# Optimization experiments

Measured on AMD Instinct MI355X. Metric: run time of the kernel, lower is better.

## Reference

```python
import jax, jax.numpy as jnp
import numpy as np

B, N, DIM, H = 2, 4096, 1024, 16
LAT = 1024
CTX = N - LAT            # 3072 context tokens
SEG = 12                 # num_segments
CHUNK = CTX // SEG       # 256 tokens per segment
D = DIM // H             # 64 head dim
SCALE = D ** -0.5
LN_EPS = 1e-5
NEG = float(-np.finfo(np.float32).max)


def _split_heads(t):  # [B, N, DIM] -> [(B*H), N, D]
    return t.reshape(B, N, H, D).transpose(0, 2, 1, 3).reshape(B * H, N, D)


def _merge_heads(t):  # [(B*H), n, D] -> [B, n, DIM]
    n = t.shape[1]
    return t.reshape(B, H, n, D).transpose(0, 2, 1, 3).reshape(B, n, DIM)


def _layernorm(t, g, b):  # LN over last dim (head dim)
    mu = t.mean(-1, keepdims=True)
    var = ((t - mu) ** 2).mean(-1, keepdims=True)
    return (t - mu) * jax.lax.rsqrt(var + LN_EPS) * g + b


def _rope(t):  # rotary embedding over full head dim, half-split rotate
    pos = jnp.arange(N, dtype=jnp.float32)
    inv = 1.0 / (10000.0 ** (jnp.arange(0, D, 2, dtype=jnp.float32) / D))
    freqs = pos[:, None] * inv[None, :]          # [N, D/2]
    emb = jnp.concatenate([freqs, freqs], -1)    # [N, D]
    cos, sin = jnp.cos(emb), jnp.sin(emb)
    rot = jnp.concatenate([-t[..., D // 2:], t[..., : D // 2]], -1)
    return t * cos + rot * sin


def setup_inputs() -> dict:
    key = jax.random.key(0)
    ks = jax.random.split(key, 4)
    s = 0.02
    return {
        "x": jax.random.normal(ks[0], (B, N, DIM), jnp.float32),
        "Wq": jax.random.normal(ks[1], (DIM, DIM), jnp.float32) * s,
        "Wkv": jax.random.normal(ks[2], (DIM, DIM), jnp.float32) * s,
        "Wo": jax.random.normal(ks[3], (DIM, DIM), jnp.float32) * s,
        "bo": jnp.zeros((DIM,), jnp.float32),
        "ln_g": jnp.ones((D,), jnp.float32),
        "ln_b": jnp.zeros((D,), jnp.float32),
    }


def reference(x, Wq, Wkv, Wo, bo, ln_g, ln_b):
    q = _split_heads(x @ Wq)    # [(BH), N, D]
    kv = _split_heads(x @ Wkv)  # [(BH), N, D]
    q, kv = _rope(q), _rope(kv)

    lkv = _layernorm(kv, ln_g, ln_b)  # normalized keys/values, full seq

    q_lat = q[:, CTX:] * SCALE                                   # [(BH), LAT, D]
    q_ctx = (q[:, :CTX] * SCALE).reshape(B * H, SEG, CHUNK, D)   # segmented ctx queries
    lkv_ctx = lkv[:, :CTX].reshape(B * H, SEG, CHUNK, D)         # segmented norm'd kv

    # latent queries: full attention over all N positions, causal among latents
    lsim = jnp.einsum('bid,bjd->bij', q_lat, lkv)                # [(BH), LAT, N]
    tri = jnp.triu(jnp.ones((LAT, LAT), bool), 1)
    lat_block = jnp.where(tri, NEG, lsim[:, :, CTX:])
    lsim = jnp.concatenate([lsim[:, :, :CTX], lat_block], axis=-1)
    attn = jax.nn.softmax(lsim, axis=-1)
    out_lat = jnp.einsum('bij,bjd->bid', attn, lkv)              # [(BH), LAT, D]

    # context queries: block-diagonal segmented local attention (non-causal)
    sim_ctx = jnp.einsum('bsid,bsjd->bsij', q_ctx, lkv_ctx)      # [(BH), SEG, CHUNK, CHUNK]
    attn_ctx = jax.nn.softmax(sim_ctx, axis=-1)
    out_ctx = jnp.einsum('bsij,bsjd->bsid', attn_ctx, lkv_ctx).reshape(B * H, CTX, D)

    out = jnp.concatenate([_merge_heads(out_ctx), _merge_heads(out_lat)], axis=1)
    return out @ Wo + bo
```

## Files before the change

kernel.cpp:

```cpp
#include <hip/hip_runtime.h>
#include <math.h>

#define NB_B 2
#define NB_N 4096
#define NB_DIM 1024
#define NB_H 16
#define NB_D 64
#define NB_CTX 3072
#define NSPLIT 4
#define QSCALE 0.18033688011112042f
#define NEGF -3.0e38f

typedef __attribute__((ext_vector_type(8))) short short8;
typedef __attribute__((ext_vector_type(4))) short s4v;
typedef __attribute__((ext_vector_type(4))) float f32x4;

#if __has_builtin(__builtin_amdgcn_mfma_f32_16x16x16bf16_1k)
__device__ __forceinline__ f32x4 mfma16(s4v a, s4v b, f32x4 c) {
  return __builtin_amdgcn_mfma_f32_16x16x16bf16_1k(a, b, c, 0, 0, 0);
}
#else
__device__ __forceinline__ f32x4 mfma16(s4v a, s4v b, f32x4 c) {
  f32x4 d;
  asm volatile("v_mfma_f32_16x16x16_bf16 %0, %1, %2, %3"
               : "=v"(d) : "v"(a), "v"(b), "v"(c));
  return d;
}
#endif

__device__ __forceinline__ unsigned short f2bf(float f) {
  union { float f; unsigned u; } v; v.f = f;
  unsigned r = v.u + 0x7fffu + ((v.u >> 16) & 1u);
  return (unsigned short)(r >> 16);
}

__device__ __forceinline__ void async16(const void* g, void* l) {
  typedef const unsigned int __attribute__((address_space(1)))* gas_t;
  typedef unsigned int __attribute__((address_space(3)))* las_t;
  __builtin_amdgcn_global_load_lds((gas_t)(unsigned long long)g,
                                   (las_t)(unsigned)(unsigned long long)l,
                                   16, 0, 0);
}

__global__ __launch_bounds__(256) void k_prep(
    const float* __restrict__ x,
    const float* __restrict__ Wq, const float* __restrict__ Wkv, const float* __restrict__ Wo,
    unsigned short* __restrict__ xb, unsigned short* __restrict__ WqkvT,
    unsigned short* __restrict__ WoT, float2* __restrict__ tab)
{
  __shared__ float tile[64][65];
  const int bx = blockIdx.x, tid = threadIdx.x;
  if (bx < 2048) {
    const float4* x4 = (const float4*)x;
    ushort4* xb4 = (ushort4*)xb;
    const int n4 = (NB_B * NB_N * NB_DIM) / 4;
    for (int i = bx * 256 + tid; i < n4; i += 2048 * 256) {
      float4 v = x4[i];
      ushort4 o;
      o.x = f2bf(v.x); o.y = f2bf(v.y); o.z = f2bf(v.z); o.w = f2bf(v.w);
      xb4[i] = o;
    }
  } else if (bx < 2816) {
    int idx = bx - 2048;
    int z = idx >> 8, rem = idx & 255;
    const float* W; unsigned short* out;
    if (z == 0)      { W = Wq;  out = WqkvT; }
    else if (z == 1) { W = Wkv; out = WqkvT + 1024 * 1024; }
    else             { W = Wo;  out = WoT; }
    int c0 = (rem & 15) * 64, k0 = (rem >> 4) * 64;
    int tx = tid & 63, ty = tid >> 6;
    #pragma unroll
    for (int i = 0; i < 16; ++i) {
      int k = ty + i * 4;
      tile[k][tx] = W[(long)(k0 + k) * 1024 + c0 + tx];
    }
    __syncthreads();
    #pragma unroll
    for (int i = 0; i < 16; ++i) {
      int c = ty + i * 4;
      out[(long)(c0 + c) * 1024 + k0 + tx] = f2bf(tile[tx][c]);
    }
  } else {
    int idx = (bx - 2816) * 256 + tid;
    int n = idx >> 5, fi = idx & 31;
    float inv = exp2f(-(float)fi * (13.287712379549449f / 32.0f));
    float ang = (float)n * inv;
    float s, c;
    sincosf(ang, &s, &c);
    tab[idx] = make_float2(c, s);
  }
}

__global__ __launch_bounds__(256) void k_gemm_qkv(
    const unsigned short* __restrict__ A,
    const unsigned short* __restrict__ Bt,
    unsigned short* __restrict__ qf,
    unsigned short* __restrict__ lkvp,
    const float2* __restrict__ tab,
    const float* __restrict__ ln_g,
    const float* __restrict__ ln_b)
{
  __shared__ unsigned short As[128 * 32];
  __shared__ unsigned short Bs[128 * 32];
  const int tid = threadIdx.x;
  const int w = tid >> 6, lane = tid & 63;
  const int wr = w >> 1, wc = w & 1;
  const int quad = lane >> 4, l15 = lane & 15;
  const long tm = (long)blockIdx.y * 128, tn = (long)blockIdx.x * 128;
  const int K = 1024;

  f32x4 acc[4][4];
  #pragma unroll
  for (int i = 0; i < 4; ++i)
    #pragma unroll
    for (int j = 0; j < 4; ++j)
      acc[i][j] = (f32x4){0.f, 0.f, 0.f, 0.f};

  const unsigned short* Ag0 = A + (tm + w * 16 + (lane >> 2)) * K + (lane & 3) * 8;
  const unsigned short* Bg0 = Bt + (tn + w * 16 + (lane >> 2)) * K + (lane & 3) * 8;
  const unsigned short* Ag1 = Ag0 + (long)64 * K;
  const unsigned short* Bg1 = Bg0 + (long)64 * K;
  unsigned short* Al0 = &As[(w * 16) * 32];
  unsigned short* Al1 = &As[(64 + w * 16) * 32];
  unsigned short* Bl0 = &Bs[(w * 16) * 32];
  unsigned short* Bl1 = &Bs[(64 + w * 16) * 32];

  for (int k0 = 0; k0 < K; k0 += 32) {
    __syncthreads();
    async16(Ag0 + k0, Al0);
    async16(Ag1 + k0, Al1);
    async16(Bg0 + k0, Bl0);
    async16(Bg1 + k0, Bl1);
    __syncthreads();
    short8 af[4], bfr[4];
    #pragma unroll
    for (int i = 0; i < 4; ++i)
      af[i] = *(const short8*)&As[(wr * 64 + i * 16 + l15) * 32 + quad * 8];
    #pragma unroll
    for (int j = 0; j < 4; ++j)
      bfr[j] = *(const short8*)&Bs[(wc * 64 + j * 16 + l15) * 32 + quad * 8];
    #pragma unroll
    for (int i = 0; i < 4; ++i)
      #pragma unroll
      for (int j = 0; j < 4; ++j)
        acc[i][j] = __builtin_amdgcn_mfma_f32_16x16x32_bf16(af[i], bfr[j], acc[i][j], 0, 0, 0);
  }

  const int col_base = (int)tn + wc * 64;
  const bool is_q = col_base < 1024;
  const int hh = (col_base & 1023) >> 6;
  unsigned short* dst = is_q ? qf : lkvp;
  float g_ln[4], b_ln[4];
  #pragma unroll
  for (int j = 0; j < 4; ++j) { g_ln[j] = ln_g[j * 16 + l15]; b_ln[j] = ln_b[j * 16 + l15]; }

  const int row_base = (int)tm + wr * 64;
  #pragma unroll
  for (int i = 0; i < 4; ++i) {
    #pragma unroll
    for (int r = 0; r < 4; ++r) {
      const int row = row_base + i * 16 + quad * 4 + r;
      const int n = row & 4095, b = row >> 12;
      const float2 cs0 = tab[n * 32 + l15];
      const float2 cs1 = tab[n * 32 + 16 + l15];
      float val[4];
      #pragma unroll
      for (int j = 0; j < 4; ++j) {
        float t = acc[i][j][r], pt = acc[i][j ^ 2][r];
        float2 cs = (j & 1) ? cs1 : cs0;
        float rot = (j < 2) ? -pt : pt;
        val[j] = t * cs.x + rot * cs.y;
      }
      unsigned short* orow = dst + ((long)(b * 16 + hh) * NB_N + n) * 64;
      if (is_q) {
        #pragma unroll
        for (int j = 0; j < 4; ++j)
          orow[j * 16 + l15] = f2bf(val[j] * QSCALE);
      } else {
        float s = val[0] + val[1] + val[2] + val[3];
        #pragma unroll
        for (int o = 1; o < 16; o <<= 1) s += __shfl_xor(s, o);
        const float mu = s * 0.015625f;
        float dv[4], vs = 0.f;
        #pragma unroll
        for (int j = 0; j < 4; ++j) { dv[j] = val[j] - mu; vs += dv[j] * dv[j]; }
        #pragma unroll
        for (int o = 1; o < 16; o <<= 1) vs += __shfl_xor(vs, o);
        const float rr = rsqrtf(vs * 0.015625f + 1e-5f);
        #pragma unroll
        for (int j = 0; j < 4; ++j)
          orow[j * 16 + l15] = f2bf(dv[j] * rr * g_ln[j] + b_ln[j]);
      }
    }
  }
}

__global__ __launch_bounds__(256) void k_gemm_bt(
    const unsigned short* __restrict__ A,
    const unsigned short* __restrict__ Bt,
    float* __restrict__ C,
    const float* __restrict__ bias,
    int K, int ldc)
{
  __shared__ unsigned short As[128 * 32];
  __shared__ unsigned short Bs[128 * 32];
  const int tid = threadIdx.x;
  const int w = tid >> 6, lane = tid & 63;
  const int wr = w >> 1, wc = w & 1;
  const int quad = lane >> 4, l15 = lane & 15;
  const long tm = (long)blockIdx.y * 128, tn = (long)blockIdx.x * 128;

  f32x4 acc[4][4];
  #pragma unroll
  for (int i = 0; i < 4; ++i)
    #pragma unroll
    for (int j = 0; j < 4; ++j)
      acc[i][j] = (f32x4){0.f, 0.f, 0.f, 0.f};

  const unsigned short* Ag0 = A + (tm + w * 16 + (lane >> 2)) * K + (lane & 3) * 8;
  const unsigned short* Bg0 = Bt + (tn + w * 16 + (lane >> 2)) * K + (lane & 3) * 8;
  const unsigned short* Ag1 = Ag0 + (long)64 * K;
  const unsigned short* Bg1 = Bg0 + (long)64 * K;
  unsigned short* Al0 = &As[(w * 16) * 32];
  unsigned short* Al1 = &As[(64 + w * 16) * 32];
  unsigned short* Bl0 = &Bs[(w * 16) * 32];
  unsigned short* Bl1 = &Bs[(64 + w * 16) * 32];

  for (int k0 = 0; k0 < K; k0 += 32) {
    __syncthreads();
    async16(Ag0 + k0, Al0);
    async16(Ag1 + k0, Al1);
    async16(Bg0 + k0, Bl0);
    async16(Bg1 + k0, Bl1);
    __syncthreads();
    short8 af[4], bfr[4];
    #pragma unroll
    for (int i = 0; i < 4; ++i)
      af[i] = *(const short8*)&As[(wr * 64 + i * 16 + l15) * 32 + quad * 8];
    #pragma unroll
    for (int j = 0; j < 4; ++j)
      bfr[j] = *(const short8*)&Bs[(wc * 64 + j * 16 + l15) * 32 + quad * 8];
    #pragma unroll
    for (int i = 0; i < 4; ++i)
      #pragma unroll
      for (int j = 0; j < 4; ++j)
        acc[i][j] = __builtin_amdgcn_mfma_f32_16x16x32_bf16(af[i], bfr[j], acc[i][j], 0, 0, 0);
  }

  #pragma unroll
  for (int j = 0; j < 4; ++j) {
    const long col = tn + wc * 64 + j * 16 + l15;
    const float bv = bias ? bias[col] : 0.0f;
    #pragma unroll
    for (int i = 0; i < 4; ++i) {
      #pragma unroll
      for (int r = 0; r < 4; ++r) {
        const long row = tm + wr * 64 + i * 16 + quad * 4 + r;
        C[row * ldc + col] = acc[i][j][r] + bv;
      }
    }
  }
}

__global__ __launch_bounds__(256) void k_attn(
    const unsigned short* __restrict__ qf,
    const unsigned short* __restrict__ lkv,
    unsigned short* __restrict__ attn_out,
    float* __restrict__ Opart,
    float* __restrict__ mpart,
    float* __restrict__ lpart)
{
  __shared__ unsigned short smem[18432];
  unsigned short* QPs = smem + 9216;
  float* smf = (float*)smem;

  const int tid = threadIdx.x;
  const int w = tid >> 6, lane = tid & 63;
  const int quad = lane >> 4, l15 = lane & 15;

  const int bx = blockIdx.x;
  int bh, q0tok, kstart, kt0, kt1, q0lat, s6 = 0, qb = 0;
  bool latent;
  if (bx < 256 * NSPLIT) {
    latent = true;
    qb = bx / NSPLIT;
    s6 = bx % NSPLIT;
    bh = qb >> 3;
    q0lat = (qb & 7) * 128;
    q0tok = NB_CTX + q0lat;
    kstart = 0;
    int nkt = (NB_CTX + q0lat + 128) >> 6;
    kt0 = (s6 * nkt) / NSPLIT;
    kt1 = ((s6 + 1) * nkt) / NSPLIT;
  } else {
    latent = false;
    int idx = bx - 256 * NSPLIT;
    bh = idx / 24;
    int r2 = idx % 24;
    int seg = r2 >> 1;
    q0lat = 0;
    q0tok = seg * 256 + (r2 & 1) * 128;
    kstart = seg * 256;
    kt0 = 0; kt1 = 4;
  }

  const unsigned short* qbase = qf + ((long)bh * NB_N + q0tok) * 64;
  const unsigned short* kbase = lkv + (long)bh * NB_N * 64;

  const int skey = tid >> 3, sdc = tid & 7;

  uint4 gA, gB;
  {
    const int key0 = kstart + kt0 * 64;
    gA = *(const uint4*)(kbase + (long)(key0 + skey) * 64 + sdc * 8);
    gB = *(const uint4*)(kbase + (long)(key0 + skey + 32) * 64 + sdc * 8);
  }

  #pragma unroll
  for (int p = 0; p < 4; ++p) {
    int ci = p * 256 + tid;
    int row = ci >> 3, dc = ci & 7;
    *(uint4*)&QPs[row * 72 + dc * 8] = *(const uint4*)(qbase + row * 64 + dc * 8);
  }

  {
    unsigned short* Ks = smem;
    unsigned short* Vt = smem + 4608;
    *(uint4*)&Ks[skey * 72 + sdc * 8] = gA;
    *(uint4*)&Ks[(skey + 32) * 72 + sdc * 8] = gB;
    const unsigned short* eA = (const unsigned short*)&gA;
    const unsigned short* eB = (const unsigned short*)&gB;
    const int swA = skey ^ (sdc * 8);
    const int swB = (skey + 32) ^ (sdc * 8);
    #pragma unroll
    for (int j = 0; j < 8; ++j) {
      Vt[(sdc * 8 + j) * 72 + swA] = eA[j];
      Vt[(sdc * 8 + j) * 72 + swB] = eB[j];
    }
  }
  __syncthreads();

  short8 qfr[2][2];
  #pragma unroll
  for (int qg = 0; qg < 2; ++qg)
    #pragma unroll
    for (int kc = 0; kc < 2; ++kc)
      qfr[qg][kc] = *(const short8*)&QPs[(w * 32 + qg * 16 + l15) * 72 + kc * 32 + quad * 8];
  __syncthreads();

  f32x4 ot[2][4];
  float mi[2], li[2];
  #pragma unroll
  for (int qg = 0; qg < 2; ++qg) {
    #pragma unroll
    for (int dt = 0; dt < 4; ++dt) ot[qg][dt] = (f32x4){0.f, 0.f, 0.f, 0.f};
    mi[qg] = NEGF; li[qg] = 0.f;
  }

  for (int kt = kt0; kt < kt1; ++kt) {
    const int cur = (kt - kt0) & 1;
    unsigned short* Ks = smem + cur * 9216;
    unsigned short* Vt = Ks + 4608;
    const int key0 = kstart + kt * 64;
    const bool more = (kt + 1 < kt1);

    if (more) {
      const int key0n = key0 + 64;
      gA = *(const uint4*)(kbase + (long)(key0n + skey) * 64 + sdc * 8);
      gB = *(const uint4*)(kbase + (long)(key0n + skey + 32) * 64 + sdc * 8);
    }

    f32x4 st[2][4];
    #pragma unroll
    for (int qg = 0; qg < 2; ++qg)
      #pragma unroll
      for (int k4 = 0; k4 < 4; ++k4)
        st[qg][k4] = (f32x4){0.f, 0.f, 0.f, 0.f};
    #pragma unroll
    for (int kc = 0; kc < 2; ++kc) {
      short8 kf[4];
      #pragma unroll
      for (int k4 = 0; k4 < 4; ++k4)
        kf[k4] = *(const short8*)&Ks[(k4 * 16 + l15) * 72 + kc * 32 + quad * 8];
      #pragma unroll
      for (int qg = 0; qg < 2; ++qg)
        #pragma unroll
        for (int k4 = 0; k4 < 4; ++k4)
          st[qg][k4] = __builtin_amdgcn_mfma_f32_16x16x32_bf16(kf[k4], qfr[qg][kc], st[qg][k4], 0, 0, 0);
    }

    if (latent && key0 + 63 >= NB_CTX) {
      #pragma unroll
      for (int qg = 0; qg < 2; ++qg) {
        const int qrow = q0lat + w * 32 + qg * 16 + l15;
        #pragma unroll
        for (int k4 = 0; k4 < 4; ++k4)
          #pragma unroll
          for (int r = 0; r < 4; ++r) {
            const int kl = key0 + k4 * 16 + quad * 4 + r - NB_CTX;
            if (kl > qrow) st[qg][k4][r] = NEGF;
          }
      }
    }

    unsigned int pk[2][4][2];
    #pragma unroll
    for (int qg = 0; qg < 2; ++qg) {
      float mx = st[qg][0][0];
      #pragma unroll
      for (int k4 = 0; k4 < 4; ++k4)
        #pragma unroll
        for (int r = 0; r < 4; ++r) mx = fmaxf(mx, st[qg][k4][r]);
      mx = fmaxf(mx, __shfl_xor(mx, 16));
      mx = fmaxf(mx, __shfl_xor(mx, 32));
      const float mnew = fmaxf(mi[qg], mx);
      const float alpha = __builtin_amdgcn_exp2f(mi[qg] - mnew);
      mi[qg] = mnew;
      float rs = 0.f;
      #pragma unroll
      for (int k4 = 0; k4 < 4; ++k4) {
        unsigned int b[4];
        #pragma unroll
        for (int r = 0; r < 4; ++r) {
          float p = __builtin_amdgcn_exp2f(st[qg][k4][r] - mnew);
          unsigned int pb = __float_as_uint(p) & 0xffff0000u;
          rs += __uint_as_float(pb);
          b[r] = pb;
        }
        pk[qg][k4][0] = __builtin_amdgcn_perm(b[1], b[0], 0x07060302);
        pk[qg][k4][1] = __builtin_amdgcn_perm(b[3], b[2], 0x07060302);
      }
      rs += __shfl_xor(rs, 16);
      rs += __shfl_xor(rs, 32);
      li[qg] = li[qg] * alpha + rs;
      #pragma unroll
      for (int dt = 0; dt < 4; ++dt) {
        ot[qg][dt][0] *= alpha; ot[qg][dt][1] *= alpha;
        ot[qg][dt][2] *= alpha; ot[qg][dt][3] *= alpha;
      }
    }

    #pragma unroll
    for (int k4 = 0; k4 < 4; ++k4) {
      s4v vf[4];
      const int kb = k4 * 16 + quad * 4;
      #pragma unroll
      for (int dt = 0; dt < 4; ++dt) {
        const int row = dt * 16 + l15;
        vf[dt] = *(const s4v*)&Vt[row * 72 + (kb ^ (row & 56))];
      }
      #pragma unroll
      for (int qg = 0; qg < 2; ++qg) {
        s4v pf;
        ((unsigned int*)&pf)[0] = pk[qg][k4][0];
        ((unsigned int*)&pf)[1] = pk[qg][k4][1];
        #pragma unroll
        for (int dt = 0; dt < 4; ++dt)
          ot[qg][dt] = mfma16(vf[dt], pf, ot[qg][dt]);
      }
    }

    if (more) {
      unsigned short* Kn = smem + (cur ^ 1) * 9216;
      unsigned short* Vn = Kn + 4608;
      *(uint4*)&Kn[skey * 72 + sdc * 8] = gA;
      *(uint4*)&Kn[(skey + 32) * 72 + sdc * 8] = gB;
      const unsigned short* eA = (const unsigned short*)&gA;
      const unsigned short* eB = (const unsigned short*)&gB;
      const int swA = skey ^ (sdc * 8);
      const int swB = (skey + 32) ^ (sdc * 8);
      #pragma unroll
      for (int j = 0; j < 8; ++j) {
        Vn[(sdc * 8 + j) * 72 + swA] = eA[j];
        Vn[(sdc * 8 + j) * 72 + swB] = eB[j];
      }
    }
    __syncthreads();
  }

  if (latent && quad == 0) {
    const long pb = (long)(s6 * 256 + qb) * 128;
    #pragma unroll
    for (int qg = 0; qg < 2; ++qg) {
      mpart[pb + w * 32 + qg * 16 + l15] = mi[qg];
      lpart[pb + w * 32 + qg * 16 + l15] = li[qg];
    }
  }
  #pragma unroll
  for (int qg = 0; qg < 2; ++qg) {
    const int q = w * 32 + qg * 16 + l15;
    #pragma unroll
    for (int dt = 0; dt < 4; ++dt)
      #pragma unroll
      for (int r = 0; r < 4; ++r)
        smf[q * 68 + dt * 16 + quad * 4 + r] = ot[qg][dt][r];
    if (!latent && quad == 0) smf[q * 68 + 64] = li[qg];
  }
  __syncthreads();
  const int row = tid >> 1, half = tid & 1;
  if (latent) {
    const long pb = (long)(s6 * 256 + qb) * 128;
    float4* dst = (float4*)(Opart + (pb + row) * 64 + half * 32);
    #pragma unroll
    for (int v = 0; v < 8; ++v)
      dst[v] = *(const float4*)&smf[row * 68 + half * 32 + v * 4];
  } else {
    const int b_ = bh >> 4, h_ = bh & 15;
    const float inv = 1.0f / smf[row * 68 + 64];
    const long tok = q0tok + row;
    unsigned short* orow = attn_out + ((long)b_ * NB_N + tok) * NB_DIM + h_ * 64 + half * 32;
    #pragma unroll
    for (int v = 0; v < 8; ++v) {
      float4 t = *(const float4*)&smf[row * 68 + half * 32 + v * 4];
      ushort4 u;
      u.x = f2bf(t.x * inv); u.y = f2bf(t.y * inv);
      u.z = f2bf(t.z * inv); u.w = f2bf(t.w * inv);
      *(ushort4*)(orow + v * 4) = u;
    }
  }
}

__global__ __launch_bounds__(256) void k_combine(
    const float* __restrict__ Opart, const float* __restrict__ mpart,
    const float* __restrict__ lpart, unsigned short* __restrict__ attn_out)
{
  const int qb = blockIdx.x;
  const int bh = qb >> 3, qt = qb & 7;
  const int b = bh >> 4, h = bh & 15;
  const int row = threadIdx.x >> 1;
  const int dh = (threadIdx.x & 1) * 32;
  float m[NSPLIT], l[NSPLIT];
  float mstar = NEGF;
  #pragma unroll
  for (int s = 0; s < NSPLIT; ++s) {
    m[s] = mpart[(s * 256 + qb) * 128 + row];
    l[s] = lpart[(s * 256 + qb) * 128 + row];
    mstar = fmaxf(mstar, m[s]);
  }
  float wgt[NSPLIT]; float lsum = 0.f;
  #pragma unroll
  for (int s = 0; s < NSPLIT; ++s) {
    wgt[s] = __builtin_amdgcn_exp2f(m[s] - mstar);
    lsum += wgt[s] * l[s];
  }
  const float inv = 1.0f / lsum;
  float o[32];
  #pragma unroll
  for (int e = 0; e < 32; ++e) o[e] = 0.f;
  #pragma unroll
  for (int s = 0; s < NSPLIT; ++s) {
    const float4* Op = (const float4*)(Opart + (((long)(s * 256 + qb) * 128 + row) * 64 + dh));
    #pragma unroll
    for (int v = 0; v < 8; ++v) {
      float4 t = Op[v];
      o[v * 4 + 0] += wgt[s] * t.x; o[v * 4 + 1] += wgt[s] * t.y;
      o[v * 4 + 2] += wgt[s] * t.z; o[v * 4 + 3] += wgt[s] * t.w;
    }
  }
  const long tok = NB_CTX + qt * 128 + row;
  unsigned short* orow = attn_out + ((long)b * NB_N + tok) * NB_DIM + h * 64 + dh;
  #pragma unroll
  for (int e = 0; e < 32; e += 4) {
    ushort4 u;
    u.x = f2bf(o[e] * inv);     u.y = f2bf(o[e + 1] * inv);
    u.z = f2bf(o[e + 2] * inv); u.w = f2bf(o[e + 3] * inv);
    *(ushort4*)(orow + e) = u;
  }
}

extern "C" void kernel_launch(void* const* d_in, const int* in_sizes, int n_in,
                              void* d_out, int out_size, void* d_ws, size_t ws_size,
                              hipStream_t stream)
{
  const float* x    = (const float*)d_in[0];
  const float* Wq   = (const float*)d_in[1];
  const float* Wkv  = (const float*)d_in[2];
  const float* Wo   = (const float*)d_in[3];
  const float* bo   = (const float*)d_in[4];
  const float* ln_g = (const float*)d_in[5];
  const float* ln_b = (const float*)d_in[6];
  float* out = (float*)d_out;

  char* ws = (char*)d_ws;
  unsigned short* xb    = (unsigned short*)(ws);
  unsigned short* WqkvT = (unsigned short*)(ws + (size_t)(16 << 20));
  unsigned short* WoT   = (unsigned short*)(ws + (size_t)(20 << 20));
  float2*         tab   = (float2*)        (ws + (size_t)(22 << 20));
  unsigned short* qfb   = (unsigned short*)(ws + (size_t)(24 << 20));
  unsigned short* lkv   = (unsigned short*)(ws + (size_t)(40 << 20));
  unsigned short* aout  = (unsigned short*)(ws + (size_t)(56 << 20));
  float*          Opart = (float*)         (ws + (size_t)(72 << 20));
  float*          mpart = (float*)         (ws + (size_t)(112 << 20));
  float*          lpart = (float*)         (ws + (size_t)(113 << 20));

  hipLaunchKernelGGL(k_prep, dim3(3328), dim3(256), 0, stream,
                     x, Wq, Wkv, Wo, xb, WqkvT, WoT, tab);
  hipLaunchKernelGGL(k_gemm_qkv, dim3(16, 64), dim3(256), 0, stream,
                     xb, WqkvT, qfb, lkv, tab, ln_g, ln_b);
  hipLaunchKernelGGL(k_attn, dim3(256 * NSPLIT + 768), dim3(256), 0, stream,
                     qfb, lkv, aout, Opart, mpart, lpart);
  hipLaunchKernelGGL(k_combine, dim3(256), dim3(256), 0, stream,
                     Opart, mpart, lpart, aout);
  hipLaunchKernelGGL(k_gemm_bt, dim3(8, 64), dim3(256), 0, stream,
                     aout, WoT, out, bo, 1024, 1024);
}
```

Baseline: 298.9 us.

## Restructure attention kernel: single-buffered LDS, lazy softmax rescale, d-major partials

```diff
diff --git a/kernel.cpp b/kernel.cpp
--- a/kernel.cpp
+++ b/kernel.cpp
@@ -270,9 +270,9 @@
     float* __restrict__ mpart,
     float* __restrict__ lpart)
 {
-  __shared__ unsigned short smem[18432];
-  unsigned short* QPs = smem + 9216;
-  float* smf = (float*)smem;
+  __shared__ unsigned short smem[9216];
+  unsigned short* Ks = smem;
+  unsigned short* Vt = smem + 4608;
 
   const int tid = threadIdx.x;
   const int w = tid >> 6, lane = tid & 63;
@@ -307,46 +307,21 @@
   const unsigned short* qbase = qf + ((long)bh * NB_N + q0tok) * 64;
   const unsigned short* kbase = lkv + (long)bh * NB_N * 64;
 
-  const int skey = tid >> 3, sdc = tid & 7;
+  short8 qfr[2][2];
+  #pragma unroll
+  for (int qg = 0; qg < 2; ++qg)
+    #pragma unroll
+    for (int kc = 0; kc < 2; ++kc)
+      qfr[qg][kc] = *(const short8*)(qbase + (w * 32 + qg * 16 + l15) * 64 + kc * 32 + quad * 8);
+
+  const int kp = tid >> 3, sdc = tid & 7;
 
   uint4 gA, gB;
   {
     const int key0 = kstart + kt0 * 64;
-    gA = *(const uint4*)(kbase + (long)(key0 + skey) * 64 + sdc * 8);
-    gB = *(const uint4*)(kbase + (long)(key0 + skey + 32) * 64 + sdc * 8);
-  }
-
-  #pragma unroll
-  for (int p = 0; p < 4; ++p) {
-    int ci = p * 256 + tid;
-    int row = ci >> 3, dc = ci & 7;
-    *(uint4*)&QPs[row * 72 + dc * 8] = *(const uint4*)(qbase + row * 64 + dc * 8);
-  }
-
-  {
-    unsigned short* Ks = smem;
-    unsigned short* Vt = smem + 4608;
-    *(uint4*)&Ks[skey * 72 + sdc * 8] = gA;
-    *(uint4*)&Ks[(skey + 32) * 72 + sdc * 8] = gB;
-    const unsigned short* eA = (const unsigned short*)&gA;
-    const unsigned short* eB = (const unsigned short*)&gB;
-    const int swA = skey ^ (sdc * 8);
-    const int swB = (skey + 32) ^ (sdc * 8);
-    #pragma unroll
-    for (int j = 0; j < 8; ++j) {
-      Vt[(sdc * 8 + j) * 72 + swA] = eA[j];
-      Vt[(sdc * 8 + j) * 72 + swB] = eB[j];
-    }
-  }
-  __syncthreads();
-
-  short8 qfr[2][2];
-  #pragma unroll
-  for (int qg = 0; qg < 2; ++qg)
-    #pragma unroll
-    for (int kc = 0; kc < 2; ++kc)
-      qfr[qg][kc] = *(const short8*)&QPs[(w * 32 + qg * 16 + l15) * 72 + kc * 32 + quad * 8];
-  __syncthreads();
+    gA = *(const uint4*)(kbase + (long)(key0 + 2 * kp) * 64 + sdc * 8);
+    gB = *(const uint4*)(kbase + (long)(key0 + 2 * kp + 1) * 64 + sdc * 8);
+  }
 
   f32x4 ot[2][4];
   float mi[2], li[2];
@@ -354,20 +329,29 @@
   for (int qg = 0; qg < 2; ++qg) {
     #pragma unroll
     for (int dt = 0; dt < 4; ++dt) ot[qg][dt] = (f32x4){0.f, 0.f, 0.f, 0.f};
-    mi[qg] = NEGF; li[qg] = 0.f;
+    mi[qg] = 0.f; li[qg] = 0.f;
   }
 
   for (int kt = kt0; kt < kt1; ++kt) {
-    const int cur = (kt - kt0) & 1;
-    unsigned short* Ks = smem + cur * 9216;
-    unsigned short* Vt = Ks + 4608;
     const int key0 = kstart + kt * 64;
-    const bool more = (kt + 1 < kt1);
-
-    if (more) {
+    __syncthreads();
+    *(uint4*)&Ks[(2 * kp) * 72 + sdc * 8] = gA;
+    *(uint4*)&Ks[(2 * kp + 1) * 72 + sdc * 8] = gB;
+    {
+      const unsigned short* eA = (const unsigned short*)&gA;
+      const unsigned short* eB = (const unsigned short*)&gB;
+      #pragma unroll
+      for (int j = 0; j < 8; ++j) {
+        const int d = sdc * 8 + j;
+        const unsigned int pair = (unsigned int)eA[j] | ((unsigned int)eB[j] << 16);
+        *(unsigned int*)&Vt[d * 72 + ((2 * kp) ^ (d & 56))] = pair;
+      }
+    }
+    __syncthreads();
+    if (kt + 1 < kt1) {
       const int key0n = key0 + 64;
-      gA = *(const uint4*)(kbase + (long)(key0n + skey) * 64 + sdc * 8);
-      gB = *(const uint4*)(kbase + (long)(key0n + skey + 32) * 64 + sdc * 8);
+      gA = *(const uint4*)(kbase + (long)(key0n + 2 * kp) * 64 + sdc * 8);
+      gB = *(const uint4*)(kbase + (long)(key0n + 2 * kp + 1) * 64 + sdc * 8);
     }
 
     f32x4 st[2][4];
@@ -404,25 +388,18 @@
     }
 
     unsigned int pk[2][4][2];
+    float tmx[2], trs[2];
     #pragma unroll
     for (int qg = 0; qg < 2; ++qg) {
+      float rs = 0.f;
       float mx = st[qg][0][0];
-      #pragma unroll
-      for (int k4 = 0; k4 < 4; ++k4)
-        #pragma unroll
-        for (int r = 0; r < 4; ++r) mx = fmaxf(mx, st[qg][k4][r]);
-      mx = fmaxf(mx, __shfl_xor(mx, 16));
-      mx = fmaxf(mx, __shfl_xor(mx, 32));
-      const float mnew = fmaxf(mi[qg], mx);
-      const float alpha = __builtin_amdgcn_exp2f(mi[qg] - mnew);
-      mi[qg] = mnew;
-      float rs = 0.f;
       #pragma unroll
       for (int k4 = 0; k4 < 4; ++k4) {
         unsigned int b[4];
         #pragma unroll
         for (int r = 0; r < 4; ++r) {
-          float p = __builtin_amdgcn_exp2f(st[qg][k4][r] - mnew);
+          mx = fmaxf(mx, st[qg][k4][r]);
+          float p = __builtin_amdgcn_exp2f(st[qg][k4][r] - mi[qg]);
           unsigned int pb = __float_as_uint(p) & 0xffff0000u;
           rs += __uint_as_float(pb);
           b[r] = pb;
@@ -430,14 +407,7 @@
         pk[qg][k4][0] = __builtin_amdgcn_perm(b[1], b[0], 0x07060302);
         pk[qg][k4][1] = __builtin_amdgcn_perm(b[3], b[2], 0x07060302);
       }
-      rs += __shfl_xor(rs, 16);
-      rs += __shfl_xor(rs, 32);
-      li[qg] = li[qg] * alpha + rs;
-      #pragma unroll
-      for (int dt = 0; dt < 4; ++dt) {
-        ot[qg][dt][0] *= alpha; ot[qg][dt][1] *= alpha;
-        ot[qg][dt][2] *= alpha; ot[qg][dt][3] *= alpha;
-      }
+      tmx[qg] = mx; trs[qg] = rs;
     }
 
     #pragma unroll
@@ -460,63 +430,64 @@
       }
     }
 
-    if (more) {
-      unsigned short* Kn = smem + (cur ^ 1) * 9216;
-      unsigned short* Vn = Kn + 4608;
-      *(uint4*)&Kn[skey * 72 + sdc * 8] = gA;
-      *(uint4*)&Kn[(skey + 32) * 72 + sdc * 8] = gB;
-      const unsigned short* eA = (const unsigned short*)&gA;
-      const unsigned short* eB = (const unsigned short*)&gB;
-      const int swA = skey ^ (sdc * 8);
-      const int swB = (skey + 32) ^ (sdc * 8);
-      #pragma unroll
-      for (int j = 0; j < 8; ++j) {
-        Vn[(sdc * 8 + j) * 72 + swA] = eA[j];
-        Vn[(sdc * 8 + j) * 72 + swB] = eB[j];
-      }
-    }
-    __syncthreads();
-  }
-
-  if (latent && quad == 0) {
-    const long pb = (long)(s6 * 256 + qb) * 128;
     #pragma unroll
     for (int qg = 0; qg < 2; ++qg) {
-      mpart[pb + w * 32 + qg * 16 + l15] = mi[qg];
-      lpart[pb + w * 32 + qg * 16 + l15] = li[qg];
-    }
-  }
-  #pragma unroll
-  for (int qg = 0; qg < 2; ++qg) {
-    const int q = w * 32 + qg * 16 + l15;
-    #pragma unroll
-    for (int dt = 0; dt < 4; ++dt)
-      #pragma unroll
-      for (int r = 0; r < 4; ++r)
-        smf[q * 68 + dt * 16 + quad * 4 + r] = ot[qg][dt][r];
-    if (!latent && quad == 0) smf[q * 68 + 64] = li[qg];
-  }
+      float rs = trs[qg];
+      rs += __shfl_xor(rs, 16);
+      rs += __shfl_xor(rs, 32);
+      float mx = tmx[qg];
+      mx = fmaxf(mx, __shfl_xor(mx, 16));
+      mx = fmaxf(mx, __shfl_xor(mx, 32));
+      const float mnew = fmaxf(mi[qg], mx);
+      const float c = __builtin_amdgcn_exp2f(mi[qg] - mnew);
+      mi[qg] = mnew;
+      li[qg] = (li[qg] + rs) * c;
+      #pragma unroll
+      for (int dt = 0; dt < 4; ++dt) {
+        ot[qg][dt][0] *= c; ot[qg][dt][1] *= c;
+        ot[qg][dt][2] *= c; ot[qg][dt][3] *= c;
+      }
+    }
+  }
+
   __syncthreads();
-  const int row = tid >> 1, half = tid & 1;
   if (latent) {
-    const long pb = (long)(s6 * 256 + qb) * 128;
-    float4* dst = (float4*)(Opart + (pb + row) * 64 + half * 32);
-    #pragma unroll
-    for (int v = 0; v < 8; ++v)
-      dst[v] = *(const float4*)&smf[row * 68 + half * 32 + v * 4];
+    const long pb = (long)(s6 * 256 + qb);
+    if (quad == 0) {
+      #pragma unroll
+      for (int qg = 0; qg < 2; ++qg) {
+        mpart[pb * 128 + w * 32 + qg * 16 + l15] = mi[qg];
+        lpart[pb * 128 + w * 32 + qg * 16 + l15] = li[qg];
+      }
+    }
+    float* obase = Opart + pb * 8192;
+    #pragma unroll
+    for (int qg = 0; qg < 2; ++qg) {
+      const int q = w * 32 + qg * 16 + l15;
+      #pragma unroll
+      for (int dt = 0; dt < 4; ++dt)
+        #pragma unroll
+        for (int r = 0; r < 4; ++r)
+          obase[(dt * 16 + quad * 4 + r) * 128 + q] = ot[qg][dt][r];
+    }
   } else {
+    #pragma unroll
+    for (int qg = 0; qg < 2; ++qg) {
+      const float inv = 1.0f / li[qg];
+      const int q = w * 32 + qg * 16 + l15;
+      #pragma unroll
+      for (int dt = 0; dt < 4; ++dt)
+        #pragma unroll
+        for (int r = 0; r < 4; ++r)
+          smem[q * 72 + dt * 16 + quad * 4 + r] = f2bf(ot[qg][dt][r] * inv);
+    }
+    __syncthreads();
+    const int qrow = tid >> 1, half = tid & 1;
     const int b_ = bh >> 4, h_ = bh & 15;
-    const float inv = 1.0f / smf[row * 68 + 64];
-    const long tok = q0tok + row;
-    unsigned short* orow = attn_out + ((long)b_ * NB_N + tok) * NB_DIM + h_ * 64 + half * 32;
-    #pragma unroll
-    for (int v = 0; v < 8; ++v) {
-      float4 t = *(const float4*)&smf[row * 68 + half * 32 + v * 4];
-      ushort4 u;
-      u.x = f2bf(t.x * inv); u.y = f2bf(t.y * inv);
-      u.z = f2bf(t.z * inv); u.w = f2bf(t.w * inv);
-      *(ushort4*)(orow + v * 4) = u;
-    }
+    unsigned short* orow = attn_out + ((long)b_ * NB_N + q0tok + qrow) * NB_DIM + h_ * 64 + half * 32;
+    #pragma unroll
+    for (int v = 0; v < 4; ++v)
+      *(uint4*)(orow + v * 8) = *(const uint4*)&smem[qrow * 72 + half * 32 + v * 8];
   }
 }
 
@@ -524,48 +495,72 @@
     const float* __restrict__ Opart, const float* __restrict__ mpart,
     const float* __restrict__ lpart, unsigned short* __restrict__ attn_out)
 {
+  __shared__ unsigned short lds[9216];
   const int qb = blockIdx.x;
   const int bh = qb >> 3, qt = qb & 7;
   const int b = bh >> 4, h = bh & 15;
-  const int row = threadIdx.x >> 1;
-  const int dh = (threadIdx.x & 1) * 32;
-  float m[NSPLIT], l[NSPLIT];
-  float mstar = NEGF;
+  const int t = threadIdx.x;
+  const int qq = t & 31;
+  const int dg = t >> 5;
+
+  float m[NSPLIT][4], l[NSPLIT][4];
+  float mstar[4];
+  #pragma unroll
+  for (int qi = 0; qi < 4; ++qi) mstar[qi] = NEGF;
   #pragma unroll
   for (int s = 0; s < NSPLIT; ++s) {
-    m[s] = mpart[(s * 256 + qb) * 128 + row];
-    l[s] = lpart[(s * 256 + qb) * 128 + row];
-    mstar = fmaxf(mstar, m[s]);
-  }
-  float wgt[NSPLIT]; float lsum = 0.f;
+    #pragma unroll
+    for (int qi = 0; qi < 4; ++qi) {
+      m[s][qi] = mpart[(s * 256 + qb) * 128 + qq * 4 + qi];
+      l[s][qi] = lpart[(s * 256 + qb) * 128 + qq * 4 + qi];
+      mstar[qi] = fmaxf(mstar[qi], m[s][qi]);
+    }
+  }
+  float inv[4];
+  #pragma unroll
+  for (int qi = 0; qi < 4; ++qi) {
+    float lsum = 0.f;
+    #pragma unroll
+    for (int s = 0; s < NSPLIT; ++s)
+      lsum += __builtin_amdgcn_exp2f(m[s][qi] - mstar[qi]) * l[s][qi];
+    inv[qi] = 1.0f / lsum;
+  }
+
+  float o[8][4];
+  #pragma unroll
+  for (int dd = 0; dd < 8; ++dd)
+    #pragma unroll
+    for (int qi = 0; qi < 4; ++qi) o[dd][qi] = 0.f;
   #pragma unroll
   for (int s = 0; s < NSPLIT; ++s) {
-    wgt[s] = __builtin_amdgcn_exp2f(m[s] - mstar);
-    lsum += wgt[s] * l[s];
-  }
-  const float inv = 1.0f / lsum;
-  float o[32];
-  #pragma unroll
-  for (int e = 0; e < 32; ++e) o[e] = 0.f;
-  #pragma unroll
-  for (int s = 0; s < NSPLIT; ++s) {
-    const float4* Op = (const float4*)(Opart + (((long)(s * 256 + qb) * 128 + row) * 64 + dh));
-    #pragma unroll
-    for (int v = 0; v < 8; ++v) {
-      float4 t = Op[v];
-      o[v * 4 + 0] += wgt[s] * t.x; o[v * 4 + 1] += wgt[s] * t.y;
-      o[v * 4 + 2] += wgt[s] * t.z; o[v * 4 + 3] += wgt[s] * t.w;
-    }
-  }
-  const long tok = NB_CTX + qt * 128 + row;
-  unsigned short* orow = attn_out + ((long)b * NB_N + tok) * NB_DIM + h * 64 + dh;
-  #pragma unroll
-  for (int e = 0; e < 32; e += 4) {
-    ushort4 u;
-    u.x = f2bf(o[e] * inv);     u.y = f2bf(o[e + 1] * inv);
-    u.z = f2bf(o[e + 2] * inv); u.w = f2bf(o[e + 3] * inv);
-    *(ushort4*)(orow + e) = u;
-  }
+    float wgt[4];
+    #pragma unroll
+    for (int qi = 0; qi < 4; ++qi)
+      wgt[qi] = __builtin_amdgcn_exp2f(m[s][qi] - mstar[qi]);
+    const float* base = Opart + (long)(s * 256 + qb) * 8192;
+    #pragma unroll
+    for (int dd = 0; dd < 8; ++dd) {
+      float4 v = *(const float4*)(base + (dg * 8 + dd) * 128 + qq * 4);
+      o[dd][0] += wgt[0] * v.x; o[dd][1] += wgt[1] * v.y;
+      o[dd][2] += wgt[2] * v.z; o[dd][3] += wgt[3] * v.w;
+    }
+  }
+  #pragma unroll
+  for (int qi = 0; qi < 4; ++qi) {
+    ushort4 u0, u1;
+    u0.x = f2bf(o[0][qi] * inv[qi]); u0.y = f2bf(o[1][qi] * inv[qi]);
+    u0.z = f2bf(o[2][qi] * inv[qi]); u0.w = f2bf(o[3][qi] * inv[qi]);
+    u1.x = f2bf(o[4][qi] * inv[qi]); u1.y = f2bf(o[5][qi] * inv[qi]);
+    u1.z = f2bf(o[6][qi] * inv[qi]); u1.w = f2bf(o[7][qi] * inv[qi]);
+    *(ushort4*)&lds[(qq * 4 + qi) * 72 + dg * 8] = u0;
+    *(ushort4*)&lds[(qq * 4 + qi) * 72 + dg * 8 + 4] = u1;
+  }
+  __syncthreads();
+  const int qrow = t >> 1, half = t & 1;
+  unsigned short* orow = attn_out + ((long)b * NB_N + NB_CTX + qt * 128 + qrow) * NB_DIM + h * 64 + half * 32;
+  #pragma unroll
+  for (int v = 0; v < 4; ++v)
+    *(uint4*)(orow + v * 8) = *(const uint4*)&lds[qrow * 72 + half * 32 + v * 8];
 }
 
 extern "C" void kernel_launch(void* const* d_in, const int* in_sizes, int n_in,
```

After: 276.3 us. 7.6% less time.
